# Performance work log

Measured on AMD Instinct MI355X. Metric: run time of the kernel, lower is better.

The kernel has to match this reference:

```python
import jax, jax.numpy as jnp
import numpy as np

N = 200000      # number of nodes / samples
D = 256         # embedding_dim
K = 20          # n_clusters


def setup_inputs() -> dict:
    key = jax.random.key(0)
    k1, k2 = jax.random.split(key)
    embeddings = jax.random.normal(k1, (N, D), dtype=jnp.float32)
    # indicator P has orthonormal-ish columns in the original (top-k eigenvectors
    # of ZZ^T); random values are fine for a correctness baseline of the math.
    indicator = jax.random.normal(k2, (N, K), dtype=jnp.float32)
    return {"embeddings": embeddings, "indicator": indicator}


def reference(embeddings, indicator):
    # Jc = tr(Z Z^T) - tr(P^T Z Z^T P)
    # tr(Z Z^T) = sum(Z * Z)
    term1 = jnp.sum(embeddings * embeddings)
    # tr(P^T Z Z^T P) = || Z^T P ||_F^2 ; Z^T P is [D, K] (tiny), avoids N x N gram.
    ztp = jnp.einsum('nd,nk->dk', embeddings, indicator)
    term2 = jnp.sum(ztp * ztp)
    return term1 - term2
```

## Files before the change

kernel.cpp:

```cpp
#include <hip/hip_runtime.h>

#define NN 200000
#define DD 256
#define KK 20


#define STAGE_LOAD(s, zv, Q0, Q1, Q2, Q3, Q4)                              \
  {                                                                        \
    int j_ = base + ((s) << 2) + w;                                        \
    if (j_ > NN - 1) j_ = 0;        \
    zv = Zr[(size_t)j_ * (DD / 4) + lane];                                 \
    int ru_ = __builtin_amdgcn_readfirstlane(j_);                          \
    const float4* pp_ = (const float4*)(P + (size_t)ru_ * KK);             \
    Q0 = pp_[0]; Q1 = pp_[1]; Q2 = pp_[2]; Q3 = pp_[3]; Q4 = pp_[4];       \
  }

#define STAGE_COMPUTE(zv, Q0, Q1, Q2, Q3, Q4)                              \
  {                                                                        \
    float zz_[4] = {zv.x, zv.y, zv.z, zv.w};                               \
    float pv_[KK] = {Q0.x, Q0.y, Q0.z, Q0.w, Q1.x, Q1.y, Q1.z, Q1.w,       \
                     Q2.x, Q2.y, Q2.z, Q2.w, Q3.x, Q3.y, Q3.z, Q3.w,       \
                     Q4.x, Q4.y, Q4.z, Q4.w};                              \
    t1 += zz_[0] * zz_[0] + zz_[1] * zz_[1];                               \
    t1 += zz_[2] * zz_[2] + zz_[3] * zz_[3];                               \
    _Pragma("unroll") for (int k_ = 0; k_ < KK; ++k_) {                    \
      _Pragma("unroll") for (int c_ = 0; c_ < 4; ++c_)                     \
          acc[k_][c_] += zz_[c_] * pv_[k_];                                \
    }                                                                      \
  }

__global__ __launch_bounds__(256, 2) void egac_main(
    const float* __restrict__ Z, const float* __restrict__ P,
    float* __restrict__ ztp_part, float* __restrict__ t1_part, int chunk) {
  const int t = threadIdx.x;
  const int lane = t & 63;
  const int w = t >> 6;
  const int b = blockIdx.x;
  const int base = b * chunk;
  const int nst = chunk >> 2;

  float acc[KK][4];
#pragma unroll
  for (int k = 0; k < KK; ++k)
#pragma unroll
    for (int c = 0; c < 4; ++c) acc[k][c] = 0.f;
  float t1 = 0.f;

  const float4* Zr = (const float4*)Z;

  float4 zA, A0, A1, A2, A3, A4;
  float4 zB, B0, B1, B2, B3, B4;
  float4 zC, C0, C1, C2, C3, C4;

  STAGE_LOAD(0, zA, A0, A1, A2, A3, A4);
  STAGE_LOAD(1, zB, B0, B1, B2, B3, B4);

  int s = 0;
  const int m_end = (nst - 2) / 3;
  for (int m = 0; m < m_end; ++m) {
    STAGE_LOAD(s + 2, zC, C0, C1, C2, C3, C4);
    STAGE_COMPUTE(zA, A0, A1, A2, A3, A4);
    STAGE_LOAD(s + 3, zA, A0, A1, A2, A3, A4);
    STAGE_COMPUTE(zB, B0, B1, B2, B3, B4);
    STAGE_LOAD(s + 4, zB, B0, B1, B2, B3, B4);
    STAGE_COMPUTE(zC, C0, C1, C2, C3, C4);
    s += 3;
  }
  STAGE_COMPUTE(zA, A0, A1, A2, A3, A4);
  STAGE_COMPUTE(zB, B0, B1, B2, B3, B4);

  __shared__ float red[KK][DD];
  __shared__ float wsum[4];
  for (int ph = 0; ph < 4; ++ph) {
    if (w == ph) {
      if (ph == 0) {
#pragma unroll
        for (int k = 0; k < KK; ++k)
          ((float4*)&red[k][0])[lane] =
              make_float4(acc[k][0], acc[k][1], acc[k][2], acc[k][3]);
      } else {
#pragma unroll
        for (int k = 0; k < KK; ++k) {
          float4 r = ((float4*)&red[k][0])[lane];
          r.x += acc[k][0]; r.y += acc[k][1];
          r.z += acc[k][2]; r.w += acc[k][3];
          ((float4*)&red[k][0])[lane] = r;
        }
      }
    }
    __syncthreads();
  }

#pragma unroll
  for (int off = 32; off > 0; off >>= 1) t1 += __shfl_xor(t1, off, 64);
  if (lane == 0) wsum[w] = t1;
  __syncthreads();

  float4* dst = (float4*)(ztp_part + (size_t)b * (KK * DD));
  const float4* src = (const float4*)&red[0][0];
#pragma unroll
  for (int i = 0; i < (KK * DD) / (4 * 256); ++i)
    dst[i * 256 + t] = src[i * 256 + t];
  if (t == 0) t1_part[b] = wsum[0] + wsum[1] + wsum[2] + wsum[3];
}

__global__ __launch_bounds__(512) void egac_reduce(
    const float* __restrict__ ztp_part, const float* __restrict__ t1_part,
    float* __restrict__ out, int nb) {
  __shared__ float red[16][32];
  const int t = threadIdx.x;
  const int el = t & 31;
  const int ps = t >> 5;
  const int e = blockIdx.x * 32 + el;

  float s = 0.f;
  for (int p = ps; p < nb; p += 16) s += ztp_part[(size_t)p * (KK * DD) + e];
  red[ps][el] = s;
  __syncthreads();
  for (int sh = 8; sh >= 1; sh >>= 1) {
    if (ps < sh) red[ps][el] += red[ps + sh][el];
    __syncthreads();
  }
  if (t == 0) {
    float ssq = 0.f;
#pragma unroll
    for (int i = 0; i < 32; ++i) {
      float v = red[0][i];
      ssq += v * v;
    }
    atomicAdd(out, -ssq);
  }

  if (blockIdx.x == 0) {
    float v = 0.f;
    for (int i = t; i < nb; i += 512) v += t1_part[i];
#pragma unroll
    for (int off = 32; off > 0; off >>= 1) v += __shfl_xor(v, off, 64);
    __shared__ float w2[8];
    if ((t & 63) == 0) w2[t >> 6] = v;
    __syncthreads();
    if (t == 0) {
      float tt = 0.f;
#pragma unroll
      for (int i = 0; i < 8; ++i) tt += w2[i];
      atomicAdd(out, tt);
    }
  }
}

extern "C" void kernel_launch(void* const* d_in, const int* in_sizes, int n_in,
                              void* d_out, int out_size, void* d_ws,
                              size_t ws_size, hipStream_t stream) {
  const float* Z = (const float*)d_in[0];
  const float* P = (const float*)d_in[1];
  float* out = (float*)d_out;

  int nb = 1000;
  size_t need = (size_t)nb * (KK * DD) * sizeof(float) + (size_t)nb * sizeof(float);
  if (ws_size < need) nb = 250;
  int chunk = NN / nb;

  float* ztp_part = (float*)d_ws;
  float* t1_part = (float*)d_ws + (size_t)nb * KK * DD;

  hipMemsetAsync(d_out, 0, sizeof(float), stream);
  egac_main<<<nb, 256, 0, stream>>>(Z, P, ztp_part, t1_part, chunk);
  egac_reduce<<<160, 512, 0, stream>>>(ztp_part, t1_part, out, nb);
}
```

Baseline: 321.1 us.

## Stage indicator rows in LDS per block and reuse shared memory for reduction

```diff
diff --git a/kernel.cpp b/kernel.cpp
--- a/kernel.cpp
+++ b/kernel.cpp
@@ -3,41 +3,52 @@
 #define NN 200000
 #define DD 256
 #define KK 20
+#define CHUNK 200
+#define NB (NN / CHUNK)
 
 
-#define STAGE_LOAD(s, zv, Q0, Q1, Q2, Q3, Q4)                              \
-  {                                                                        \
-    int j_ = base + ((s) << 2) + w;                                        \
-    if (j_ > NN - 1) j_ = 0;        \
-    zv = Zr[(size_t)j_ * (DD / 4) + lane];                                 \
-    int ru_ = __builtin_amdgcn_readfirstlane(j_);                          \
-    const float4* pp_ = (const float4*)(P + (size_t)ru_ * KK);             \
-    Q0 = pp_[0]; Q1 = pp_[1]; Q2 = pp_[2]; Q3 = pp_[3]; Q4 = pp_[4];       \
+#define SLOAD(i, zv) zv = Zr[(size_t)((((i) << 2) + w) * 64 + lane)];
+
+#define SCOMP(i, zv)                                                        \
+  {                                                                         \
+    const float4* pr_ = (const float4*)(smem + ((((i) << 2) + w) * KK));    \
+    float4 p0_ = pr_[0], p1_ = pr_[1], p2_ = pr_[2], p3_ = pr_[3],          \
+           p4_ = pr_[4];                                                    \
+    float zz_[4] = {zv.x, zv.y, zv.z, zv.w};                                \
+    float pv_[KK] = {p0_.x, p0_.y, p0_.z, p0_.w, p1_.x, p1_.y, p1_.z,       \
+                     p1_.w, p2_.x, p2_.y, p2_.z, p2_.w, p3_.x, p3_.y,       \
+                     p3_.z, p3_.w, p4_.x, p4_.y, p4_.z, p4_.w};             \
+    t1 += zz_[0] * zz_[0] + zz_[1] * zz_[1];                                \
+    t1 += zz_[2] * zz_[2] + zz_[3] * zz_[3];                                \
+    _Pragma("unroll") for (int k_ = 0; k_ < KK; ++k_) {                     \
+      _Pragma("unroll") for (int c_ = 0; c_ < 4; ++c_)                      \
+          acc[k_][c_] += zz_[c_] * pv_[k_];                                 \
+    }                                                                       \
   }
 
-#define STAGE_COMPUTE(zv, Q0, Q1, Q2, Q3, Q4)                              \
-  {                                                                        \
-    float zz_[4] = {zv.x, zv.y, zv.z, zv.w};                               \
-    float pv_[KK] = {Q0.x, Q0.y, Q0.z, Q0.w, Q1.x, Q1.y, Q1.z, Q1.w,       \
-                     Q2.x, Q2.y, Q2.z, Q2.w, Q3.x, Q3.y, Q3.z, Q3.w,       \
-                     Q4.x, Q4.y, Q4.z, Q4.w};                              \
-    t1 += zz_[0] * zz_[0] + zz_[1] * zz_[1];                               \
-    t1 += zz_[2] * zz_[2] + zz_[3] * zz_[3];                               \
-    _Pragma("unroll") for (int k_ = 0; k_ < KK; ++k_) {                    \
-      _Pragma("unroll") for (int c_ = 0; c_ < 4; ++c_)                     \
-          acc[k_][c_] += zz_[c_] * pv_[k_];                                \
-    }                                                                      \
-  }
-
-__global__ __launch_bounds__(256, 2) void egac_main(
+__global__ __launch_bounds__(256, 3) void egac_main(
     const float* __restrict__ Z, const float* __restrict__ P,
-    float* __restrict__ ztp_part, float* __restrict__ t1_part, int chunk) {
+    float* __restrict__ ztp_part, float* __restrict__ t1_part) {
   const int t = threadIdx.x;
   const int lane = t & 63;
   const int w = t >> 6;
   const int b = blockIdx.x;
-  const int base = b * chunk;
-  const int nst = chunk >> 2;
+  const int base = b * CHUNK;
+
+  __shared__ float smem[KK * DD];
+  __shared__ float wsum[4];
+
+  {
+    const float4* Psrc = (const float4*)(P + (size_t)base * KK);
+    float4* pl4 = (float4*)smem;
+    const int n4 = CHUNK * KK / 4;
+#pragma unroll
+    for (int i = 0; i < 4; ++i) {
+      int idx = t + i * 256;
+      if (idx < n4) pl4[idx] = Psrc[idx];
+    }
+  }
+  __syncthreads();
 
   float acc[KK][4];
 #pragma unroll
@@ -46,31 +57,33 @@
     for (int c = 0; c < 4; ++c) acc[k][c] = 0.f;
   float t1 = 0.f;
 
-  const float4* Zr = (const float4*)Z;
+  const float4* Zr = (const float4*)(Z + (size_t)base * DD);
+  const int nit = CHUNK / 4;
 
-  float4 zA, A0, A1, A2, A3, A4;
-  float4 zB, B0, B1, B2, B3, B4;
-  float4 zC, C0, C1, C2, C3, C4;
-
-  STAGE_LOAD(0, zA, A0, A1, A2, A3, A4);
-  STAGE_LOAD(1, zB, B0, B1, B2, B3, B4);
+  float4 zA, zB, zC;
+  SLOAD(0, zA);
+  SLOAD(1, zB);
 
   int s = 0;
-  const int m_end = (nst - 2) / 3;
+  const int m_end = (nit - 2) / 3;
   for (int m = 0; m < m_end; ++m) {
-    STAGE_LOAD(s + 2, zC, C0, C1, C2, C3, C4);
-    STAGE_COMPUTE(zA, A0, A1, A2, A3, A4);
-    STAGE_LOAD(s + 3, zA, A0, A1, A2, A3, A4);
-    STAGE_COMPUTE(zB, B0, B1, B2, B3, B4);
-    STAGE_LOAD(s + 4, zB, B0, B1, B2, B3, B4);
-    STAGE_COMPUTE(zC, C0, C1, C2, C3, C4);
+    SLOAD(s + 2, zC);
+    SCOMP(s, zA);
+    SLOAD(s + 3, zA);
+    SCOMP(s + 1, zB);
+    SLOAD(s + 4, zB);
+    SCOMP(s + 2, zC);
     s += 3;
   }
-  STAGE_COMPUTE(zA, A0, A1, A2, A3, A4);
-  STAGE_COMPUTE(zB, B0, B1, B2, B3, B4);
+  for (int i = s; i < nit; ++i) {
+    if (i + 2 < nit) SLOAD(i + 2, zC);
+    SCOMP(i, zA);
+    zA = zB;
+    zB = zC;
+  }
 
-  __shared__ float red[KK][DD];
-  __shared__ float wsum[4];
+  __syncthreads();
+  float(*red)[DD] = (float(*)[DD])smem;
   for (int ph = 0; ph < 4; ++ph) {
     if (w == ph) {
       if (ph == 0) {
@@ -82,8 +95,10 @@
 #pragma unroll
         for (int k = 0; k < KK; ++k) {
           float4 r = ((float4*)&red[k][0])[lane];
-          r.x += acc[k][0]; r.y += acc[k][1];
-          r.z += acc[k][2]; r.w += acc[k][3];
+          r.x += acc[k][0];
+          r.y += acc[k][1];
+          r.z += acc[k][2];
+          r.w += acc[k][3];
           ((float4*)&red[k][0])[lane] = r;
         }
       }
@@ -155,15 +170,10 @@
   const float* P = (const float*)d_in[1];
   float* out = (float*)d_out;
 
-  int nb = 1000;
-  size_t need = (size_t)nb * (KK * DD) * sizeof(float) + (size_t)nb * sizeof(float);
-  if (ws_size < need) nb = 250;
-  int chunk = NN / nb;
-
   float* ztp_part = (float*)d_ws;
-  float* t1_part = (float*)d_ws + (size_t)nb * KK * DD;
+  float* t1_part = (float*)d_ws + (size_t)NB * KK * DD;
 
   hipMemsetAsync(d_out, 0, sizeof(float), stream);
-  egac_main<<<nb, 256, 0, stream>>>(Z, P, ztp_part, t1_part, chunk);
-  egac_reduce<<<160, 512, 0, stream>>>(ztp_part, t1_part, out, nb);
+  egac_main<<<NB, 256, 0, stream>>>(Z, P, ztp_part, t1_part);
+  egac_reduce<<<160, 512, 0, stream>>>(ztp_part, t1_part, out, NB);
 }
```

Measured after the change: 322.2 us. No clear change (+0.3%).
